# Kernel tuning notes

Hardware: AMD Instinct MI355X
Metric: run time of the kernel (lower is better)

The kernel has to match this reference:

```python
import jax, jax.numpy as jnp
import numpy as np

EMBED_DIM = 512
N_HEAD = 8
HEAD_DIM = EMBED_DIM // N_HEAD  # 64
B, S = 2, 4096
NEG_FILL = -1e20


def setup_inputs() -> dict:
    key = jax.random.key(0)
    ks = jax.random.split(key, 9)
    inp = {
        "key": jax.random.normal(ks[0], (B, S, EMBED_DIM), jnp.float32),
        "query": jax.random.normal(ks[1], (B, S, EMBED_DIM), jnp.float32),
        "value": jax.random.normal(ks[2], (B, S, EMBED_DIM), jnp.float32),
        "mask": jax.random.randint(ks[3], (1, 1, S, S), 0, 2, jnp.int32),
        # per-head projections (shared across heads, as in the source: a single
        # d x d nn.Linear applied to the last dim of [B,S,H,d])
        "Wq": jax.random.normal(ks[4], (HEAD_DIM, HEAD_DIM), jnp.float32) / np.sqrt(HEAD_DIM),
        "Wk": jax.random.normal(ks[5], (HEAD_DIM, HEAD_DIM), jnp.float32) / np.sqrt(HEAD_DIM),
        "Wv": jax.random.normal(ks[6], (HEAD_DIM, HEAD_DIM), jnp.float32) / np.sqrt(HEAD_DIM),
        "Wo": jax.random.normal(ks[7], (EMBED_DIM, EMBED_DIM), jnp.float32) / np.sqrt(EMBED_DIM),
        "bo": jax.random.normal(ks[8], (EMBED_DIM,), jnp.float32) * 0.01,
    }
    return inp


def reference(key, query, value, mask, Wq, Wk, Wv, Wo, bo):
    b, sq, e = query.shape
    skv = key.shape[1]
    h, d = N_HEAD, HEAD_DIM
    # split heads: [B, S, H, d]
    q = query.reshape(b, sq, h, d) @ Wq.T
    k = key.reshape(b, skv, h, d) @ Wk.T
    v = value.reshape(b, skv, h, d) @ Wv.T
    # scores: [B, H, Sq, Skv]
    scores = jnp.einsum("bqhd,bkhd->bhqk", q, k)
    # source masks BEFORE scaling: fill -1e20 then divide by sqrt(d)
    scores = jnp.where(mask == 0, NEG_FILL, scores)
    scores = scores / np.sqrt(d).astype(np.float32)
    attn = jax.nn.softmax(scores, axis=-1)
    ctx = jnp.einsum("bhqk,bkhd->bqhd", attn, v)  # [B, Sq, H, d]
    concat = ctx.reshape(b, sq, h * d)
    return concat @ Wo.T + bo
```

## Files before the change

kernel.cpp:

```cpp
#include <hip/hip_runtime.h>

typedef __bf16 bf16;
typedef __attribute__((ext_vector_type(8)))  bf16     bf16x8;
typedef __attribute__((ext_vector_type(4)))  bf16     bf16x4;
typedef __attribute__((ext_vector_type(16))) float    f32x16;
typedef __attribute__((ext_vector_type(4)))  float    f32x4;
typedef __attribute__((ext_vector_type(4)))  unsigned uint4v;
typedef __attribute__((ext_vector_type(2)))  unsigned uint2v;

#define SLEN 4096
#define HDIM 64
#define EMB 512
#define NTILES 64
#define SCALE_LOG2E 0.1803336100254854f

__device__ __forceinline__ f32x16 mfma32(bf16x8 a, bf16x8 b, f32x16 c) {
  return __builtin_amdgcn_mfma_f32_32x32x16_bf16(a, b, c, 0, 0, 0);
}

__device__ __forceinline__ void cp16(const void* g, const void* l) {
  __builtin_amdgcn_global_load_lds(
      (__attribute__((address_space(1))) unsigned int*)(unsigned long long)g,
      (__attribute__((address_space(3))) unsigned int*)(unsigned int)(unsigned long long)l,
      16, 0, 0);
}

__device__ __forceinline__ unsigned pk2(float a, float b) {
  unsigned short ua = __builtin_bit_cast(unsigned short, (bf16)a);
  unsigned short ub = __builtin_bit_cast(unsigned short, (bf16)b);
  return (unsigned)ua | ((unsigned)ub << 16);
}

__global__ __launch_bounds__(256, 2) void proj_qkv(
    const float* __restrict__ key, const float* __restrict__ query, const float* __restrict__ value,
    const float* __restrict__ Wq, const float* __restrict__ Wk, const float* __restrict__ Wv,
    bf16* __restrict__ Qb, bf16* __restrict__ Kb, bf16* __restrict__ VT)
{
  __shared__ __align__(16) bf16 tile[128][64];
  const int tid = threadIdx.x, w = tid >> 6, lane = tid & 63, l31 = lane & 31, lh = lane >> 5;
  const int r0 = blockIdx.x * 128;
  const int m0 = r0 + w * 32;

  #pragma unroll
  for (int p = 0; p < 3; ++p) {
    const float* X = (p == 0) ? query : (p == 1) ? key : value;
    const float* W = (p == 0) ? Wq    : (p == 1) ? Wk  : Wv;

    bf16x8 af[4];
    {
      const float* xr = X + (size_t)(m0 + l31) * 64 + 8 * lh;
      #pragma unroll
      for (int c = 0; c < 4; ++c) {
        f32x4 lo = *(const f32x4*)(xr + c * 16);
        f32x4 hi = *(const f32x4*)(xr + c * 16 + 4);
        bf16x8 v;
        #pragma unroll
        for (int j = 0; j < 4; ++j) { v[j] = (bf16)lo[j]; v[4 + j] = (bf16)hi[j]; }
        af[c] = v;
      }
    }
    bf16x8 bfr[2][4];
    #pragma unroll
    for (int nb = 0; nb < 2; ++nb) {
      const float* wr = W + (size_t)(l31 + 32 * nb) * 64 + 8 * lh;
      #pragma unroll
      for (int c = 0; c < 4; ++c) {
        f32x4 lo = *(const f32x4*)(wr + c * 16);
        f32x4 hi = *(const f32x4*)(wr + c * 16 + 4);
        bf16x8 v;
        #pragma unroll
        for (int j = 0; j < 4; ++j) { v[j] = (bf16)lo[j]; v[4 + j] = (bf16)hi[j]; }
        bfr[nb][c] = v;
      }
    }
    f32x16 a0, a1;
    #pragma unroll
    for (int r = 0; r < 16; ++r) { a0[r] = 0.f; a1[r] = 0.f; }
    #pragma unroll
    for (int c = 0; c < 4; ++c) {
      a0 = mfma32(af[c], bfr[0][c], a0);
      a1 = mfma32(af[c], bfr[1][c], a1);
    }

    const float qs = (p == 0) ? SCALE_LOG2E : 1.0f;
    __syncthreads();
    #pragma unroll
    for (int r = 0; r < 16; ++r) {
      const int row = w * 32 + (r & 3) + 8 * (r >> 2) + 4 * lh;
      tile[row][l31]      = (bf16)(a0[r] * qs);
      tile[row][l31 + 32] = (bf16)(a1[r] * qs);
    }
    __syncthreads();

    if (p < 2) {
      bf16* OUT = p ? Kb : Qb;
      const int rloc = tid >> 1, hf = tid & 1;
      const int rg = r0 + rloc, bs = rg >> 3, h = rg & 7, b = bs >> 12, sidx = bs & 4095;
      bf16* dst = OUT + (((size_t)(b * 8 + h) * SLEN + sidx) * 64 + hf * 32);
      const bf16* srcp = &tile[rloc][hf * 32];
      #pragma unroll
      for (int u = 0; u < 4; ++u) *(uint4v*)(dst + u * 8) = *(const uint4v*)(srcp + u * 8);
    } else {
      const int h = tid >> 5, d0 = tid & 31;
      const int b = blockIdx.x >> 8, s0 = (blockIdx.x * 16) & 4095;
      #pragma unroll
      for (int dh = 0; dh < 2; ++dh) {
        const int dd = d0 + 32 * dh;
        unsigned pk4[8];
        #pragma unroll
        for (int t2 = 0; t2 < 8; ++t2) {
          unsigned short ua = __builtin_bit_cast(unsigned short, tile[(2 * t2) * 8 + h][dd]);
          unsigned short ub = __builtin_bit_cast(unsigned short, tile[(2 * t2 + 1) * 8 + h][dd]);
          pk4[t2] = (unsigned)ua | ((unsigned)ub << 16);
        }
        bf16* dst = VT + ((size_t)(b * 8 + h) * 64 + dd) * SLEN + s0;
        uint4v A; A[0] = pk4[0]; A[1] = pk4[1]; A[2] = pk4[2]; A[3] = pk4[3];
        uint4v Bv; Bv[0] = pk4[4]; Bv[1] = pk4[5]; Bv[2] = pk4[6]; Bv[3] = pk4[7];
        *(uint4v*)(dst) = A;
        *(uint4v*)(dst + 8) = Bv;
      }
    }
  }
}

__device__ __forceinline__ unsigned nib_compress(unsigned x) {
  x = (x | (x >> 4)) & 0x00FF00FFu;
  x = (x | (x >> 8)) & 0x0000FFFFu;
  return x;
}
__global__ void pack_mask(const int* __restrict__ mask, unsigned* __restrict__ MW)
{
  const int w = threadIdx.x >> 6, lane = threadIdx.x & 63;
  const int q = blockIdx.x * 4 + w;
  const int* row = mask + (size_t)q * SLEN;
  unsigned long long mine = 0ull;
  #pragma unroll 4
  for (int i = 0; i < 64; ++i) {
    unsigned long long b = __ballot(row[i * 64 + lane] != 0);
    if (i == lane) mine = b;
  }
  const unsigned lo = (unsigned)mine, hi = (unsigned)(mine >> 32);
  const unsigned w0 = nib_compress(lo & 0x0F0F0F0Fu)        | (nib_compress(hi & 0x0F0F0F0Fu) << 16);
  const unsigned w1 = nib_compress((lo >> 4) & 0x0F0F0F0Fu) | (nib_compress((hi >> 4) & 0x0F0F0F0Fu) << 16);
  MW[(size_t)lane * SLEN + q] = w0;
  MW[(size_t)NTILES * SLEN + (size_t)lane * SLEN + q] = w1;
}

__global__ void wo_split(const float* __restrict__ Wo, bf16* __restrict__ WH, bf16* __restrict__ WL)
{
  const int i = (blockIdx.x * 256 + threadIdx.x) * 4;
  f32x4 v = *(const f32x4*)(Wo + i);
  bf16x4 h, l;
  #pragma unroll
  for (int j = 0; j < 4; ++j) { h[j] = (bf16)v[j]; l[j] = (bf16)(v[j] - (float)h[j]); }
  *(bf16x4*)(WH + i) = h;
  *(bf16x4*)(WL + i) = l;
}

__global__ __launch_bounds__(256, 3) void attn_kernel(
    const bf16* __restrict__ Qb, const bf16* __restrict__ Kb, const bf16* __restrict__ VT,
    const unsigned* __restrict__ MW,
    bf16* __restrict__ ctxh, bf16* __restrict__ ctxl)
{
  __shared__ __align__(16) unsigned char smem[49152];

  const int tid = threadIdx.x, w = tid >> 6, lane = tid & 63, l31 = lane & 31, lh = lane >> 5;
  const int qg = w & 1, kc = w >> 1;
  const int bh = blockIdx.x >> 6, qt = blockIdx.x & 63;
  const int q0 = qt * 64;
  const int qrow = q0 + qg * 32 + l31;
  const int lh4 = 4 * lh;
  const int kcs = kc << 4;

  const bf16* qp = Qb + ((size_t)bh * SLEN + qrow) * HDIM + 8 * lh;
  const bf16x8 qf0 = *(const bf16x8*)(qp);
  const bf16x8 qf1 = *(const bf16x8*)(qp + 16);
  const bf16x8 qf2 = *(const bf16x8*)(qp + 32);
  const bf16x8 qf3 = *(const bf16x8*)(qp + 48);

  const int f0 = 2 * w, f1 = 2 * w + 1;
  const bf16* kp0 = Kb + ((size_t)bh * SLEN + (f0 >> 2) * 32 + l31) * HDIM + (f0 & 3) * 16 + 8 * lh;
  const bf16* kp1 = Kb + ((size_t)bh * SLEN + (f1 >> 2) * 32 + l31) * HDIM + (f1 & 3) * 16 + 8 * lh;
  const bf16* vp0 = VT + ((size_t)bh * HDIM + (f0 >> 2) * 32 + l31) * SLEN + (f0 & 3) * 16 + 8 * lh;
  const bf16* vp1 = VT + ((size_t)bh * HDIM + (f1 >> 2) * 32 + l31) * SLEN + (f1 & 3) * 16 + 8 * lh;

  unsigned char* sA = smem;
  unsigned char* sB = smem + 16384;
  unsigned char* sC = smem + 32768;
  const int fko = f0 * 1024;
  const int fvo = 8192 + f0 * 1024;
  const int lb = lane * 16;
  const int kroff = kc * 4096 + lb;
  const int vroff = 8192 + kc * 2048 + lb;

  f32x16 o0, o1, Z16;
  #pragma unroll
  for (int r = 0; r < 16; ++r) { o0[r] = 0.f; o1[r] = 0.f; Z16[r] = 0.f; }
  float la0 = 0.f, la1 = 0.f, la2 = 0.f, la3 = 0.f;

  const unsigned* mp = MW + (size_t)lh * NTILES * SLEN + qrow;

  cp16(kp0, sA + fko); cp16(kp1, sA + fko + 1024);
  cp16(vp0, sA + fvo); cp16(vp1, sA + fvo + 1024);
  kp0 += 4096; kp1 += 4096; vp0 += 64; vp1 += 64;
  unsigned mwc = *mp;
  mp += SLEN;
  cp16(kp0, sB + fko); cp16(kp1, sB + fko + 1024);
  cp16(vp0, sB + fvo); cp16(vp1, sB + fvo + 1024);
  kp0 += 4096; kp1 += 4096; vp0 += 64; vp1 += 64;

  for (int t = 0; t < NTILES; ++t) {
    asm volatile("s_waitcnt vmcnt(4)" ::: "memory");
    __builtin_amdgcn_sched_barrier(0);
    __builtin_amdgcn_s_barrier();

    const unsigned mwn = *mp;
    mp += SLEN;

    cp16(kp0, sC + fko); cp16(kp1, sC + fko + 1024);
    cp16(vp0, sC + fvo); cp16(vp1, sC + fvo + 1024);
    kp0 += 4096; kp1 += 4096; vp0 += 64; vp1 += 64;

    const unsigned char* kr = sA + kroff;
    const unsigned char* vr = sA + vroff;

    __builtin_amdgcn_s_setprio(1);
    f32x16 s = mfma32(*(const bf16x8*)(kr), qf0, Z16);
    s = mfma32(*(const bf16x8*)(kr + 1024), qf1, s);
    s = mfma32(*(const bf16x8*)(kr + 2048), qf2, s);
    s = mfma32(*(const bf16x8*)(kr + 3072), qf3, s);
    __builtin_amdgcn_s_setprio(0);

    const unsigned mwk = mwc >> kcs;
    float p[16];
    #pragma unroll
    for (int r = 0; r < 16; ++r) {
      float e = __builtin_amdgcn_exp2f(s[r]);
      unsigned kbit = (unsigned)(((int)(mwk << (31 - r))) >> 31);
      e = __builtin_bit_cast(float, __builtin_bit_cast(unsigned, e) & kbit);
      p[r] = e;
      if ((r & 3) == 0) la0 += e; else if ((r & 3) == 1) la1 += e;
      else if ((r & 3) == 2) la2 += e; else la3 += e;
    }

    bf16x8 bp0, bp1;
    {
      unsigned Wa = pk2(p[0], p[1]), Wb = pk2(p[2], p[3]);
      unsigned Wc = pk2(p[4], p[5]), Wd = pk2(p[6], p[7]);
      uint2v s02 = __builtin_amdgcn_permlane32_swap(Wa, Wc, false, false);
      uint2v s13 = __builtin_amdgcn_permlane32_swap(Wb, Wd, false, false);
      uint4v fw; fw[0] = s02[0]; fw[1] = s13[0]; fw[2] = s02[1]; fw[3] = s13[1];
      bp0 = __builtin_bit_cast(bf16x8, fw);
    }
    {
      unsigned Wa = pk2(p[8], p[9]), Wb = pk2(p[10], p[11]);
      unsigned Wc = pk2(p[12], p[13]), Wd = pk2(p[14], p[15]);
      uint2v s02 = __builtin_amdgcn_permlane32_swap(Wa, Wc, false, false);
      uint2v s13 = __builtin_amdgcn_permlane32_swap(Wb, Wd, false, false);
      uint4v fw; fw[0] = s02[0]; fw[1] = s13[0]; fw[2] = s02[1]; fw[3] = s13[1];
      bp1 = __builtin_bit_cast(bf16x8, fw);
    }

    __builtin_amdgcn_s_setprio(1);
    o0 = mfma32(*(const bf16x8*)(vr), bp0, o0);
    o0 = mfma32(*(const bf16x8*)(vr + 1024), bp1, o0);
    o1 = mfma32(*(const bf16x8*)(vr + 4096), bp0, o1);
    o1 = mfma32(*(const bf16x8*)(vr + 4096 + 1024), bp1, o1);
    __builtin_amdgcn_s_setprio(0);

    { unsigned char* tmp_ = sA; sA = sB; sB = sC; sC = tmp_; }
    mwc = mwn;
  }

  asm volatile("s_waitcnt vmcnt(0)" ::: "memory");
  __builtin_amdgcn_s_barrier();

  float plsum = (la0 + la1) + (la2 + la3);
  plsum += __shfl_xor(plsum, 32);

  float* POl = (float*)smem;
  float* PLl = (float*)(smem + 16384);

  if (w >= 2) {
    const int pw = w - 2;
    #pragma unroll
    for (int r = 0; r < 16; ++r) {
      POl[(pw * 32 + r) * 64 + lane]      = o0[r];
      POl[(pw * 32 + 16 + r) * 64 + lane] = o1[r];
    }
    PLl[pw * 64 + lane] = plsum;
  }
  __syncthreads();
  if (w < 2) {
    #pragma unroll
    for (int r = 0; r < 16; ++r) {
      o0[r] += POl[(w * 32 + r) * 64 + lane];
      o1[r] += POl[(w * 32 + 16 + r) * 64 + lane];
    }
    plsum += PLl[w * 64 + lane];
    const float inv = 1.f / plsum;
    #pragma unroll
    for (int r = 0; r < 16; ++r) { o0[r] *= inv; o1[r] *= inv; }
  }
  __syncthreads();

  bf16* Tr = (bf16*)(smem + 17408);
  if (w < 2) {
    #pragma unroll
    for (int r = 0; r < 16; ++r) {
      const int dr = (r & 3) + 8 * (r >> 2) + lh4;
      Tr[(w * 32 + l31) * 72 + dr]      = (bf16)o0[r];
      Tr[(w * 32 + l31) * 72 + 32 + dr] = (bf16)o1[r];
    }
  }
  __syncthreads();
  if (tid < 128) {
    const int rloc = tid >> 1, hf = tid & 1;
    bf16* dst = ctxh + ((size_t)bh * SLEN + q0 + rloc) * 64 + hf * 32;
    const bf16* srcp = Tr + rloc * 72 + hf * 32;
    #pragma unroll
    for (int u = 0; u < 4; ++u) *(uint4v*)(dst + u * 8) = *(const uint4v*)(srcp + u * 8);
  }
  __syncthreads();
  if (w < 2) {
    #pragma unroll
    for (int r = 0; r < 16; ++r) {
      const int dr = (r & 3) + 8 * (r >> 2) + lh4;
      const float h0 = (float)(bf16)o0[r];
      const float h1 = (float)(bf16)o1[r];
      Tr[(w * 32 + l31) * 72 + dr]      = (bf16)(o0[r] - h0);
      Tr[(w * 32 + l31) * 72 + 32 + dr] = (bf16)(o1[r] - h1);
    }
  }
  __syncthreads();
  if (tid < 128) {
    const int rloc = tid >> 1, hf = tid & 1;
    bf16* dst = ctxl + ((size_t)bh * SLEN + q0 + rloc) * 64 + hf * 32;
    const bf16* srcp = Tr + rloc * 72 + hf * 32;
    #pragma unroll
    for (int u = 0; u < 4; ++u) *(uint4v*)(dst + u * 8) = *(const uint4v*)(srcp + u * 8);
  }
}

__global__ __launch_bounds__(256, 2) void out_proj(
    const bf16* __restrict__ CH, const bf16* __restrict__ CL,
    const bf16* __restrict__ WH, const bf16* __restrict__ WL,
    const float* __restrict__ bo, float* __restrict__ out)
{
  __shared__ __align__(16) bf16 Af[2][4][4][64][8];
  const int tid = threadIdx.x, w = tid >> 6, lane = tid & 63, l31 = lane & 31, lh = lane >> 5;
  const int mt = blockIdx.x >> 3, nt = blockIdx.x & 7;
  const int bs0 = mt * 128, n0 = nt * 64;
  const int b = bs0 >> 12, sbase = bs0 & 4095;

  f32x16 a0, a1;
  #pragma unroll
  for (int r = 0; r < 16; ++r) { a0[r] = 0.f; a1[r] = 0.f; }

  for (int kk = 0; kk < 8; ++kk) {
    __syncthreads();
    #pragma unroll
    for (int qq = 0; qq < 8; ++qq) {
      const int fid = w * 8 + qq, pl = fid >> 4, mb = (fid >> 2) & 3, c = fid & 3;
      const bf16* src = (pl ? CL : CH) +
          ((size_t)(b * 8 + kk) * SLEN + sbase + 32 * mb + l31) * 64 + 16 * c + 8 * lh;
      cp16(src, &Af[pl][mb][c][0][0]);
    }
    __syncthreads();

    bf16x8 bh0[4], bl0[4], bh1[4], bl1[4], ah[4], al[4];
    #pragma unroll
    for (int c = 0; c < 4; ++c) {
      const size_t o0off = (size_t)(n0 + l31) * EMB + kk * 64 + 16 * c + 8 * lh;
      const size_t o1off = (size_t)(n0 + l31 + 32) * EMB + kk * 64 + 16 * c + 8 * lh;
      bh0[c] = *(const bf16x8*)(WH + o0off);
      bl0[c] = *(const bf16x8*)(WL + o0off);
      bh1[c] = *(const bf16x8*)(WH + o1off);
      bl1[c] = *(const bf16x8*)(WL + o1off);
      ah[c] = *(const bf16x8*)(&Af[0][w][c][lane][0]);
      al[c] = *(const bf16x8*)(&Af[1][w][c][lane][0]);
    }
    #pragma unroll
    for (int c = 0; c < 4; ++c) {
      a0 = mfma32(ah[c], bh0[c], a0);
      a0 = mfma32(ah[c], bl0[c], a0);
      a0 = mfma32(al[c], bh0[c], a0);
      a1 = mfma32(ah[c], bh1[c], a1);
      a1 = mfma32(ah[c], bl1[c], a1);
      a1 = mfma32(al[c], bh1[c], a1);
    }
  }

  const float bv0 = bo[n0 + l31], bv1 = bo[n0 + l31 + 32];
  #pragma unroll
  for (int r = 0; r < 16; ++r) {
    const int row = bs0 + w * 32 + (r & 3) + 8 * (r >> 2) + 4 * lh;
    out[(size_t)row * EMB + n0 + l31]      = a0[r] + bv0;
    out[(size_t)row * EMB + n0 + l31 + 32] = a1[r] + bv1;
  }
}

extern "C" void kernel_launch(void* const* d_in, const int* in_sizes, int n_in,
                              void* d_out, int out_size, void* d_ws, size_t ws_size,
                              hipStream_t stream)
{
  (void)in_sizes; (void)n_in; (void)out_size; (void)ws_size;
  const float* key   = (const float*)d_in[0];
  const float* query = (const float*)d_in[1];
  const float* value = (const float*)d_in[2];
  const int*   mask  = (const int*)d_in[3];
  const float* Wq    = (const float*)d_in[4];
  const float* Wk    = (const float*)d_in[5];
  const float* Wv    = (const float*)d_in[6];
  const float* Wo    = (const float*)d_in[7];
  const float* bo    = (const float*)d_in[8];
  float* out = (float*)d_out;

  char* ws = (char*)d_ws;
  bf16* Qb = (bf16*)(ws);
  bf16* Kb = (bf16*)(ws + (8ull  << 20));
  bf16* VT = (bf16*)(ws + (16ull << 20));
  unsigned* MW = (unsigned*)(ws + (24ull << 20));
  bf16* CH = (bf16*)(ws + (26ull << 20));
  bf16* CL = (bf16*)(ws + (34ull << 20));
  bf16* WH = (bf16*)(ws + (42ull << 20));
  bf16* WL = (bf16*)(ws + (42ull << 20) + (512ull << 10));

  proj_qkv<<<512, 256, 0, stream>>>(key, query, value, Wq, Wk, Wv, Qb, Kb, VT);
  pack_mask<<<1024, 256, 0, stream>>>(mask, MW);
  wo_split<<<256, 256, 0, stream>>>(Wo, WH, WL);
  attn_kernel<<<1024, 256, 0, stream>>>(Qb, Kb, VT, MW, CH, CL);
  out_proj<<<512, 256, 0, stream>>>(CH, CL, WH, WL, bo, out);
}
```

Baseline: 268.0 us.

## Restructure attention to 2-wave blocks with 32-key tiles, double buffering and no split-K

Attention blocks shrink from four waves, which split the keys into two halves and then reduce partial outputs through shared memory, to two waves that each own 32 query rows and walk all keys. Each step now loads a 32-key tile into a double buffer with two barriers per tile, instead of a triple-buffered 64-key tile with one barrier. Block ids are remapped across heads, which may change L2 locality. The cross-wave reduction is gone and occupancy per CU may rise, at the cost of twice as many barriers and smaller tiles per step.

```diff
diff --git a/kernel.cpp b/kernel.cpp
--- a/kernel.cpp
+++ b/kernel.cpp
@@ -157,20 +157,19 @@
   *(bf16x4*)(WL + i) = l;
 }
 
-__global__ __launch_bounds__(256, 3) void attn_kernel(
+__global__ __launch_bounds__(128, 4) void attn_kernel(
     const bf16* __restrict__ Qb, const bf16* __restrict__ Kb, const bf16* __restrict__ VT,
     const unsigned* __restrict__ MW,
     bf16* __restrict__ ctxh, bf16* __restrict__ ctxl)
 {
-  __shared__ __align__(16) unsigned char smem[49152];
+  __shared__ __align__(16) unsigned char smem[16384];
 
   const int tid = threadIdx.x, w = tid >> 6, lane = tid & 63, l31 = lane & 31, lh = lane >> 5;
-  const int qg = w & 1, kc = w >> 1;
-  const int bh = blockIdx.x >> 6, qt = blockIdx.x & 63;
-  const int q0 = qt * 64;
-  const int qrow = q0 + qg * 32 + l31;
+  const int logical = (blockIdx.x & 7) * 128 + (blockIdx.x >> 3);
+  const int bh = logical >> 6, qt = logical & 63;
+  const int q0w = qt * 64 + w * 32;
+  const int qrow = q0w + l31;
   const int lh4 = 4 * lh;
-  const int kcs = kc << 4;
 
   const bf16* qp = Qb + ((size_t)bh * SLEN + qrow) * HDIM + 8 * lh;
   const bf16x8 qf0 = *(const bf16x8*)(qp);
@@ -178,168 +177,135 @@
   const bf16x8 qf2 = *(const bf16x8*)(qp + 32);
   const bf16x8 qf3 = *(const bf16x8*)(qp + 48);
 
-  const int f0 = 2 * w, f1 = 2 * w + 1;
-  const bf16* kp0 = Kb + ((size_t)bh * SLEN + (f0 >> 2) * 32 + l31) * HDIM + (f0 & 3) * 16 + 8 * lh;
-  const bf16* kp1 = Kb + ((size_t)bh * SLEN + (f1 >> 2) * 32 + l31) * HDIM + (f1 & 3) * 16 + 8 * lh;
-  const bf16* vp0 = VT + ((size_t)bh * HDIM + (f0 >> 2) * 32 + l31) * SLEN + (f0 & 3) * 16 + 8 * lh;
-  const bf16* vp1 = VT + ((size_t)bh * HDIM + (f1 >> 2) * 32 + l31) * SLEN + (f1 & 3) * 16 + 8 * lh;
-
-  unsigned char* sA = smem;
-  unsigned char* sB = smem + 16384;
-  unsigned char* sC = smem + 32768;
-  const int fko = f0 * 1024;
-  const int fvo = 8192 + f0 * 1024;
+  const bf16* kp0 = Kb + ((size_t)bh * SLEN + l31) * HDIM + (2 * w) * 16 + 8 * lh;
+  const bf16* kp1 = kp0 + 16;
+  const bf16* vp0 = VT + ((size_t)bh * HDIM + w * 32 + l31) * SLEN + 8 * lh;
+  const bf16* vp1 = vp0 + 16;
+
+  const int fk = 2 * w * 1024;
+  const int fv = 4096 + 2 * w * 1024;
   const int lb = lane * 16;
-  const int kroff = kc * 4096 + lb;
-  const int vroff = 8192 + kc * 2048 + lb;
 
   f32x16 o0, o1, Z16;
   #pragma unroll
   for (int r = 0; r < 16; ++r) { o0[r] = 0.f; o1[r] = 0.f; Z16[r] = 0.f; }
   float la0 = 0.f, la1 = 0.f, la2 = 0.f, la3 = 0.f;
 
+#define STAGE(BUF) { \
+  cp16(kp0, smem + (BUF) * 8192 + fk); cp16(kp1, smem + (BUF) * 8192 + fk + 1024); \
+  cp16(vp0, smem + (BUF) * 8192 + fv); cp16(vp1, smem + (BUF) * 8192 + fv + 1024); \
+  kp0 += 2048; kp1 += 2048; vp0 += 32; vp1 += 32; \
+}
+
+#define TILEC(BUF, MWORD, SH) { \
+  const unsigned char* kr = smem + (BUF) * 8192 + lb; \
+  __builtin_amdgcn_s_setprio(1); \
+  f32x16 s = mfma32(*(const bf16x8*)(kr), qf0, Z16); \
+  s = mfma32(*(const bf16x8*)(kr + 1024), qf1, s); \
+  s = mfma32(*(const bf16x8*)(kr + 2048), qf2, s); \
+  s = mfma32(*(const bf16x8*)(kr + 3072), qf3, s); \
+  __builtin_amdgcn_s_setprio(0); \
+  const unsigned mwk = (MWORD) >> (SH); \
+  float p[16]; \
+  _Pragma("unroll") \
+  for (int r = 0; r < 16; ++r) { \
+    float e = __builtin_amdgcn_exp2f(s[r]); \
+    unsigned kbit = (unsigned)(((int)(mwk << (31 - r))) >> 31); \
+    e = __builtin_bit_cast(float, __builtin_bit_cast(unsigned, e) & kbit); \
+    p[r] = e; \
+    if ((r & 3) == 0) la0 += e; else if ((r & 3) == 1) la1 += e; \
+    else if ((r & 3) == 2) la2 += e; else la3 += e; \
+  } \
+  bf16x8 bp0, bp1; \
+  { unsigned Wa = pk2(p[0], p[1]), Wb = pk2(p[2], p[3]); \
+    unsigned Wc = pk2(p[4], p[5]), Wd = pk2(p[6], p[7]); \
+    uint2v s02 = __builtin_amdgcn_permlane32_swap(Wa, Wc, false, false); \
+    uint2v s13 = __builtin_amdgcn_permlane32_swap(Wb, Wd, false, false); \
+    uint4v fw; fw[0] = s02[0]; fw[1] = s13[0]; fw[2] = s02[1]; fw[3] = s13[1]; \
+    bp0 = __builtin_bit_cast(bf16x8, fw); } \
+  { unsigned Wa = pk2(p[8], p[9]), Wb = pk2(p[10], p[11]); \
+    unsigned Wc = pk2(p[12], p[13]), Wd = pk2(p[14], p[15]); \
+    uint2v s02 = __builtin_amdgcn_permlane32_swap(Wa, Wc, false, false); \
+    uint2v s13 = __builtin_amdgcn_permlane32_swap(Wb, Wd, false, false); \
+    uint4v fw; fw[0] = s02[0]; fw[1] = s13[0]; fw[2] = s02[1]; fw[3] = s13[1]; \
+    bp1 = __builtin_bit_cast(bf16x8, fw); } \
+  const unsigned char* vr = kr + 4096; \
+  __builtin_amdgcn_s_setprio(1); \
+  o0 = mfma32(*(const bf16x8*)(vr), bp0, o0); \
+  o0 = mfma32(*(const bf16x8*)(vr + 1024), bp1, o0); \
+  o1 = mfma32(*(const bf16x8*)(vr + 2048), bp0, o1); \
+  o1 = mfma32(*(const bf16x8*)(vr + 3072), bp1, o1); \
+  __builtin_amdgcn_s_setprio(0); \
+}
+
+#define SYNC_STAGED \
+  asm volatile("s_waitcnt vmcnt(4)" ::: "memory"); \
+  __builtin_amdgcn_sched_barrier(0); \
+  __builtin_amdgcn_s_barrier(); \
+  __builtin_amdgcn_sched_barrier(0);
+
+#define SYNC_READ_DONE \
+  __builtin_amdgcn_sched_barrier(0); \
+  __builtin_amdgcn_s_barrier(); \
+  __builtin_amdgcn_sched_barrier(0);
+
   const unsigned* mp = MW + (size_t)lh * NTILES * SLEN + qrow;
 
-  cp16(kp0, sA + fko); cp16(kp1, sA + fko + 1024);
-  cp16(vp0, sA + fvo); cp16(vp1, sA + fvo + 1024);
-  kp0 += 4096; kp1 += 4096; vp0 += 64; vp1 += 64;
+  STAGE(0)
   unsigned mwc = *mp;
-  mp += SLEN;
-  cp16(kp0, sB + fko); cp16(kp1, sB + fko + 1024);
-  cp16(vp0, sB + fvo); cp16(vp1, sB + fvo + 1024);
-  kp0 += 4096; kp1 += 4096; vp0 += 64; vp1 += 64;
-
-  for (int t = 0; t < NTILES; ++t) {
-    asm volatile("s_waitcnt vmcnt(4)" ::: "memory");
-    __builtin_amdgcn_sched_barrier(0);
-    __builtin_amdgcn_s_barrier();
-
-    const unsigned mwn = *mp;
-    mp += SLEN;
-
-    cp16(kp0, sC + fko); cp16(kp1, sC + fko + 1024);
-    cp16(vp0, sC + fvo); cp16(vp1, sC + fvo + 1024);
-    kp0 += 4096; kp1 += 4096; vp0 += 64; vp1 += 64;
-
-    const unsigned char* kr = sA + kroff;
-    const unsigned char* vr = sA + vroff;
-
-    __builtin_amdgcn_s_setprio(1);
-    f32x16 s = mfma32(*(const bf16x8*)(kr), qf0, Z16);
-    s = mfma32(*(const bf16x8*)(kr + 1024), qf1, s);
-    s = mfma32(*(const bf16x8*)(kr + 2048), qf2, s);
-    s = mfma32(*(const bf16x8*)(kr + 3072), qf3, s);
-    __builtin_amdgcn_s_setprio(0);
-
-    const unsigned mwk = mwc >> kcs;
-    float p[16];
-    #pragma unroll
-    for (int r = 0; r < 16; ++r) {
-      float e = __builtin_amdgcn_exp2f(s[r]);
-      unsigned kbit = (unsigned)(((int)(mwk << (31 - r))) >> 31);
-      e = __builtin_bit_cast(float, __builtin_bit_cast(unsigned, e) & kbit);
-      p[r] = e;
-      if ((r & 3) == 0) la0 += e; else if ((r & 3) == 1) la1 += e;
-      else if ((r & 3) == 2) la2 += e; else la3 += e;
-    }
-
-    bf16x8 bp0, bp1;
-    {
-      unsigned Wa = pk2(p[0], p[1]), Wb = pk2(p[2], p[3]);
-      unsigned Wc = pk2(p[4], p[5]), Wd = pk2(p[6], p[7]);
-      uint2v s02 = __builtin_amdgcn_permlane32_swap(Wa, Wc, false, false);
-      uint2v s13 = __builtin_amdgcn_permlane32_swap(Wb, Wd, false, false);
-      uint4v fw; fw[0] = s02[0]; fw[1] = s13[0]; fw[2] = s02[1]; fw[3] = s13[1];
-      bp0 = __builtin_bit_cast(bf16x8, fw);
-    }
-    {
-      unsigned Wa = pk2(p[8], p[9]), Wb = pk2(p[10], p[11]);
-      unsigned Wc = pk2(p[12], p[13]), Wd = pk2(p[14], p[15]);
-      uint2v s02 = __builtin_amdgcn_permlane32_swap(Wa, Wc, false, false);
-      uint2v s13 = __builtin_amdgcn_permlane32_swap(Wb, Wd, false, false);
-      uint4v fw; fw[0] = s02[0]; fw[1] = s13[0]; fw[2] = s02[1]; fw[3] = s13[1];
-      bp1 = __builtin_bit_cast(bf16x8, fw);
-    }
-
-    __builtin_amdgcn_s_setprio(1);
-    o0 = mfma32(*(const bf16x8*)(vr), bp0, o0);
-    o0 = mfma32(*(const bf16x8*)(vr + 1024), bp1, o0);
-    o1 = mfma32(*(const bf16x8*)(vr + 4096), bp0, o1);
-    o1 = mfma32(*(const bf16x8*)(vr + 4096 + 1024), bp1, o1);
-    __builtin_amdgcn_s_setprio(0);
-
-    { unsigned char* tmp_ = sA; sA = sB; sB = sC; sC = tmp_; }
-    mwc = mwn;
-  }
+
+  for (int t2 = 0; t2 < 64; ++t2) {
+    STAGE(1)
+    SYNC_STAGED
+    const unsigned mwn = mp[(t2 < 63) ? SLEN : 0];
+    TILEC(0, mwc, 0)
+    SYNC_READ_DONE
+
+    STAGE(0)
+    SYNC_STAGED
+    TILEC(1, mwc, 16)
+    SYNC_READ_DONE
+
+    mwc = mwn; mp += SLEN;
+  }
+#undef STAGE
+#undef TILEC
+#undef SYNC_STAGED
+#undef SYNC_READ_DONE
 
   asm volatile("s_waitcnt vmcnt(0)" ::: "memory");
   __builtin_amdgcn_s_barrier();
 
   float plsum = (la0 + la1) + (la2 + la3);
   plsum += __shfl_xor(plsum, 32);
-
-  float* POl = (float*)smem;
-  float* PLl = (float*)(smem + 16384);
-
-  if (w >= 2) {
-    const int pw = w - 2;
-    #pragma unroll
-    for (int r = 0; r < 16; ++r) {
-      POl[(pw * 32 + r) * 64 + lane]      = o0[r];
-      POl[(pw * 32 + 16 + r) * 64 + lane] = o1[r];
-    }
-    PLl[pw * 64 + lane] = plsum;
-  }
-  __syncthreads();
-  if (w < 2) {
-    #pragma unroll
-    for (int r = 0; r < 16; ++r) {
-      o0[r] += POl[(w * 32 + r) * 64 + lane];
-      o1[r] += POl[(w * 32 + 16 + r) * 64 + lane];
-    }
-    plsum += PLl[w * 64 + lane];
-    const float inv = 1.f / plsum;
-    #pragma unroll
-    for (int r = 0; r < 16; ++r) { o0[r] *= inv; o1[r] *= inv; }
-  }
-  __syncthreads();
-
-  bf16* Tr = (bf16*)(smem + 17408);
-  if (w < 2) {
-    #pragma unroll
-    for (int r = 0; r < 16; ++r) {
-      const int dr = (r & 3) + 8 * (r >> 2) + lh4;
-      Tr[(w * 32 + l31) * 72 + dr]      = (bf16)o0[r];
-      Tr[(w * 32 + l31) * 72 + 32 + dr] = (bf16)o1[r];
-    }
-  }
-  __syncthreads();
-  if (tid < 128) {
-    const int rloc = tid >> 1, hf = tid & 1;
-    bf16* dst = ctxh + ((size_t)bh * SLEN + q0 + rloc) * 64 + hf * 32;
-    const bf16* srcp = Tr + rloc * 72 + hf * 32;
-    #pragma unroll
-    for (int u = 0; u < 4; ++u) *(uint4v*)(dst + u * 8) = *(const uint4v*)(srcp + u * 8);
-  }
-  __syncthreads();
-  if (w < 2) {
-    #pragma unroll
-    for (int r = 0; r < 16; ++r) {
-      const int dr = (r & 3) + 8 * (r >> 2) + lh4;
-      const float h0 = (float)(bf16)o0[r];
-      const float h1 = (float)(bf16)o1[r];
-      Tr[(w * 32 + l31) * 72 + dr]      = (bf16)(o0[r] - h0);
-      Tr[(w * 32 + l31) * 72 + 32 + dr] = (bf16)(o1[r] - h1);
-    }
-  }
-  __syncthreads();
-  if (tid < 128) {
-    const int rloc = tid >> 1, hf = tid & 1;
-    bf16* dst = ctxl + ((size_t)bh * SLEN + q0 + rloc) * 64 + hf * 32;
-    const bf16* srcp = Tr + rloc * 72 + hf * 32;
-    #pragma unroll
-    for (int u = 0; u < 4; ++u) *(uint4v*)(dst + u * 8) = *(const uint4v*)(srcp + u * 8);
-  }
+  const float inv = 1.f / plsum;
+  #pragma unroll
+  for (int r = 0; r < 16; ++r) { o0[r] *= inv; o1[r] *= inv; }
+
+  bf16* T = (bf16*)(smem + w * 8192);
+  const int qq = lane >> 1, hf = lane & 1;
+  bf16* dsth = ctxh + ((size_t)bh * SLEN + q0w + qq) * 64 + hf * 32;
+  bf16* dstl = ctxl + ((size_t)bh * SLEN + q0w + qq) * 64 + hf * 32;
+  const bf16* sp = T + qq * 72 + hf * 32;
+
+  #pragma unroll
+  for (int r = 0; r < 16; ++r) {
+    const int dr = (r & 3) + 8 * (r >> 2) + lh4;
+    T[l31 * 72 + dr]      = (bf16)o0[r];
+    T[l31 * 72 + 32 + dr] = (bf16)o1[r];
+  }
+  #pragma unroll
+  for (int u = 0; u < 4; ++u) *(uint4v*)(dsth + u * 8) = *(const uint4v*)(sp + u * 8);
+  #pragma unroll
+  for (int r = 0; r < 16; ++r) {
+    const int dr = (r & 3) + 8 * (r >> 2) + lh4;
+    const float h0 = (float)(bf16)o0[r];
+    const float h1 = (float)(bf16)o1[r];
+    T[l31 * 72 + dr]      = (bf16)(o0[r] - h0);
+    T[l31 * 72 + 32 + dr] = (bf16)(o1[r] - h1);
+  }
+  #pragma unroll
+  for (int u = 0; u < 4; ++u) *(uint4v*)(dstl + u * 8) = *(const uint4v*)(sp + u * 8);
 }
 
 __global__ __launch_bounds__(256, 2) void out_proj(
@@ -429,6 +395,6 @@
   proj_qkv<<<512, 256, 0, stream>>>(key, query, value, Wq, Wk, Wv, Qb, Kb, VT);
   pack_mask<<<1024, 256, 0, stream>>>(mask, MW);
   wo_split<<<256, 256, 0, stream>>>(Wo, WH, WL);
-  attn_kernel<<<1024, 256, 0, stream>>>(Qb, Kb, VT, MW, CH, CL);
+  attn_kernel<<<1024, 128, 0, stream>>>(Qb, Kb, VT, MW, CH, CL);
   out_proj<<<512, 256, 0, stream>>>(CH, CL, WH, WL, bo, out);
 }
```

Result: faster. 237.0 us (-11.6%).
